# Optimization experiments

Measured on AMD Instinct MI355X. Metric: run time of the kernel, lower is better.

## Reference

```python
import jax, jax.numpy as jnp
import numpy as np

B = 32768      # batch of ODE state evaluations
N = 64         # input_size (number of variables / per-node MLPs)
H = 64         # hidden_size
N_DISCRETE = 16  # first 16 variables use straight-through gating
HIDDEN_FLAG = True


def setup_inputs() -> dict:
    key = jax.random.key(0)
    k1, k2, k3 = jax.random.split(key, 3)
    inputs = jax.random.normal(k1, (B, N), jnp.float32)
    # Stacked per-node MLP weights: net_i is Linear(N,H,bias=False) -> ReLU -> Linear(H,1,bias=False)
    W1 = jax.random.normal(k2, (N, H, N), jnp.float32) / np.sqrt(N).astype(np.float32)
    W2 = jax.random.normal(k3, (N, H), jnp.float32) / np.sqrt(H).astype(np.float32)
    adjacency = jnp.ones((N, N), jnp.float32)  # buffer, initialized to ones
    discrete_mask = jnp.arange(N) < N_DISCRETE  # bool [N], from input_type_list
    return {"t": 0, "inputs": inputs, "W1": W1, "W2": W2,
            "adjacency": adjacency, "discrete_mask": discrete_mask}


def reference(t, inputs, W1, W2, adjacency, discrete_mask):
    # Straight-through discrete gating: y_hard - sg(y_soft) + y_soft
    y_soft = jax.nn.sigmoid(inputs)
    st = (inputs > 0).astype(inputs.dtype) - jax.lax.stop_gradient(y_soft) + y_soft
    x = jnp.where(discrete_mask[None, :], st, inputs)  # [B, N]

    # Effective per-node input mask: row i of adjacency; last node additionally
    # filtered to only its own (hidden) feature when hidden_flag is set.
    M = adjacency
    if HIDDEN_FLAG:
        one_hot_last = jnp.zeros((N,), M.dtype).at[-1].set(1.0)
        M = M.at[-1].set(M[-1] * one_hot_last)

    # Masking the input of node i by M[i] is equivalent to masking W1[i]'s input dim.
    W1m = W1 * M[:, None, :]                      # [N, H, N]
    h = jax.nn.relu(jnp.einsum('bn,ihn->bih', x, W1m))  # [B, N, H]
    out = jnp.einsum('bih,ih->bi', h, W2)               # [B, N]
    return out
```

## Files before the change

kernel.cpp:

```cpp
#include <hip/hip_runtime.h>
#include <stdint.h>


typedef __attribute__((ext_vector_type(8))) short short8;
typedef __attribute__((ext_vector_type(4))) float floatx4;

#define NN 64
#define HH 64
#define BB 32768
#define OTW 33
#define X_ELEMS (BB * NN)
#define W1_ELEMS (NN * HH * NN)

__device__ __forceinline__ unsigned short f32_to_bf16_bits(float f) {
    union { float f; unsigned int i; } c; c.f = f;
    unsigned int b = c.i;
    b += 0x7fffu + ((b >> 16) & 1u);
    return (unsigned short)(b >> 16);
}

__device__ __forceinline__ bool sniff_bf16(const void* x) {
    const int lane = threadIdx.x & 63;
    const ushort* xw = (const ushort*)x;
    const ushort a = xw[4 * lane];
    const ushort b = xw[4 * lane + 2];
    const int ea = (a >> 7) & 0xFF, eb = (b >> 7) & 0xFF;
    const int hit = ((ea >= 118 && ea <= 132) ? 1 : 0) + ((eb >= 118 && eb <= 132) ? 1 : 0);
    const unsigned long long m1 = __ballot(hit >= 1);
    const unsigned long long m2 = __ballot(hit >= 2);
    return (__popcll(m1) + __popcll(m2)) >= 64;
}

__global__ __launch_bounds__(256, 4)
void prep_kernel(const void* __restrict__ x, const void* __restrict__ w1,
                 ushort* __restrict__ xo, ushort* __restrict__ w1o)
{
    const bool is_bf16 = sniff_bf16(x);
    const long base = ((long)blockIdx.x * 256 + (long)threadIdx.x) * 8;

    if (base < X_ELEMS) {
        const bool gate = (base & 63) < 16;
        short8 v;
        if (is_bf16) {
            v = *(const short8*)((const ushort*)x + base);
            if (gate) {
                #pragma unroll
                for (int j = 0; j < 8; ++j) {
                    const unsigned short u = (unsigned short)v[j];
                    const bool pos = ((u & 0x8000u) == 0) && ((u & 0x7fffu) != 0);
                    v[j] = pos ? (short)0x3F80 : (short)0;
                }
            }
        } else {
            const float* p = (const float*)x + base;
            const float4 f0 = *(const float4*)(p);
            const float4 f1 = *(const float4*)(p + 4);
            const float vals[8] = {f0.x, f0.y, f0.z, f0.w, f1.x, f1.y, f1.z, f1.w};
            #pragma unroll
            for (int j = 0; j < 8; ++j) {
                if (gate) v[j] = (vals[j] > 0.f) ? (short)0x3F80 : (short)0;
                else      v[j] = (short)f32_to_bf16_bits(vals[j]);
            }
        }
        *(short8*)(xo + base) = v;
    } else {
        const long wb = base - X_ELEMS;
        if (wb < W1_ELEMS) {
            short8 v;
            if (is_bf16) {
                v = *(const short8*)((const ushort*)w1 + wb);
            } else {
                const float* p = (const float*)w1 + wb;
                const float4 f0 = *(const float4*)(p);
                const float4 f1 = *(const float4*)(p + 4);
                const float vals[8] = {f0.x, f0.y, f0.z, f0.w, f1.x, f1.y, f1.z, f1.w};
                #pragma unroll
                for (int j = 0; j < 8; ++j) v[j] = (short)f32_to_bf16_bits(vals[j]);
            }
            const int node = (int)(wb >> 12);
            if (node == NN - 1) {
                const int w63 = (int)(wb & 63);
                #pragma unroll
                for (int j = 0; j < 8; ++j)
                    if (w63 + j != NN - 1) v[j] = 0;
            }
            *(short8*)(w1o + wb) = v;
        }
    }
}

template<bool F32>
__device__ __forceinline__ void main_body(const ushort* __restrict__ xo,
                                          const ushort* __restrict__ w1o,
                                          const void* __restrict__ w2p,
                                          void* __restrict__ outp,
                                          float* outTile)
{
    const int tid  = threadIdx.x;
    const int wave = tid >> 6;
    const int lane = tid & 63;
    const int quad = lane >> 4;
    const int l16  = lane & 15;

    const int blk   = blockIdx.x;
    const int b0    = (blk >> 1) * 64;
    const int nhalf = blk & 1;
    const int nbase = nhalf * 32 + wave * 8;

    short8 xfrag[2][4];
    #pragma unroll
    for (int ks = 0; ks < 2; ++ks)
        #pragma unroll
        for (int nt = 0; nt < 4; ++nt)
            xfrag[ks][nt] = *(const short8*)(xo + (b0 + nt * 16 + l16) * NN + ks * 32 + quad * 8);

    short8 w[2][4];
    auto loadW1mt = [&](int node, int mt) {
        const ushort* w1n = w1o + node * (HH * NN) + (mt * 16 + l16) * NN + quad * 8;
        w[0][mt] = *(const short8*)(w1n);
        w[1][mt] = *(const short8*)(w1n + 32);
    };

    #pragma unroll
    for (int mt = 0; mt < 4; ++mt) loadW1mt(nbase, mt);

    #pragma unroll 1
    for (int np = 0; np < 8; ++np) {
        const int node = nbase + np;
        const int nextnode = (np < 7) ? (node + 1) : node;

        float w2v[4][4];
        #pragma unroll
        for (int mt = 0; mt < 4; ++mt) {
            const int idx = node * HH + mt * 16 + quad * 4;
            if (F32) {
                const float4 ww = *(const float4*)((const float*)w2p + idx);
                w2v[mt][0] = ww.x; w2v[mt][1] = ww.y; w2v[mt][2] = ww.z; w2v[mt][3] = ww.w;
            } else {
                const ushort4 ww = *(const ushort4*)((const ushort*)w2p + idx);
                union { unsigned int i; float f; } c0, c1, c2, c3;
                c0.i = ((unsigned int)ww.x) << 16; c1.i = ((unsigned int)ww.y) << 16;
                c2.i = ((unsigned int)ww.z) << 16; c3.i = ((unsigned int)ww.w) << 16;
                w2v[mt][0] = c0.f; w2v[mt][1] = c1.f; w2v[mt][2] = c2.f; w2v[mt][3] = c3.f;
            }
        }

        float psum[4] = {0.f, 0.f, 0.f, 0.f};

        #pragma unroll
        for (int mt = 0; mt < 4; ++mt) {
            floatx4 acc[4];
            #pragma unroll
            for (int nt = 0; nt < 4; ++nt) acc[nt] = (floatx4){0.f, 0.f, 0.f, 0.f};
            #pragma unroll
            for (int ks = 0; ks < 2; ++ks)
                #pragma unroll
                for (int nt = 0; nt < 4; ++nt)
                    acc[nt] = __builtin_amdgcn_mfma_f32_16x16x32_bf16(
                        w[ks][mt], xfrag[ks][nt], acc[nt], 0, 0, 0);

            loadW1mt(nextnode, mt);

            #pragma unroll
            for (int nt = 0; nt < 4; ++nt) {
                float a0 = acc[nt][0]; a0 = a0 > 0.f ? a0 : 0.f;
                float a1 = acc[nt][1]; a1 = a1 > 0.f ? a1 : 0.f;
                float a2 = acc[nt][2]; a2 = a2 > 0.f ? a2 : 0.f;
                float a3 = acc[nt][3]; a3 = a3 > 0.f ? a3 : 0.f;
                float s0 = fmaf(a0, w2v[mt][0], psum[nt]);
                float s1 = a1 * w2v[mt][1];
                s0 = fmaf(a2, w2v[mt][2], s0);
                s1 = fmaf(a3, w2v[mt][3], s1);
                psum[nt] = s0 + s1;
            }
        }

        #pragma unroll
        for (int nt = 0; nt < 4; ++nt) {
            psum[nt] += __shfl_xor(psum[nt], 16, 64);
            psum[nt] += __shfl_xor(psum[nt], 32, 64);
        }

        const float val = (quad == 0) ? psum[0] : (quad == 1) ? psum[1]
                         : (quad == 2) ? psum[2] : psum[3];
        outTile[lane * OTW + (node & 31)] = val;
    }

    __syncthreads();

    const int row = tid >> 2;
    const int q   = tid & 3;
    const float* rp = outTile + row * OTW + q * 8;
    const size_t obase = (size_t)(b0 + row) * NN + nhalf * 32 + q * 8;
    if (F32) {
        float* op = (float*)outp + obase;
        *(float4*)(op)     = make_float4(rp[0], rp[1], rp[2], rp[3]);
        *(float4*)(op + 4) = make_float4(rp[4], rp[5], rp[6], rp[7]);
    } else {
        ushort* op = (ushort*)outp + obase;
        short8 o;
        #pragma unroll
        for (int c = 0; c < 8; ++c) o[c] = (short)f32_to_bf16_bits(rp[c]);
        *(short8*)(op) = o;
    }
}

__global__ __launch_bounds__(256, 4)
void main_kernel(const void* __restrict__ xorig,
                 const ushort* __restrict__ xo, const ushort* __restrict__ w1o,
                 const void* __restrict__ w2p, void* __restrict__ outp)
{
    __shared__ float outTile[64 * OTW];
    const bool is_bf16 = sniff_bf16(xorig);
    if (is_bf16) main_body<false>(xo, w1o, w2p, outp, outTile);
    else         main_body<true >(xo, w1o, w2p, outp, outTile);
}

#define LDSW 20
template<bool F32>
__device__ __forceinline__ void run_body_fb(const void* xp, const void* w1p,
                                            const void* w2p, void* outp,
                                            float* myLds)
{
    const int tid  = threadIdx.x;
    const int wave = tid >> 6;
    const int lane = tid & 63;
    const int quad = lane >> 4;
    const int l16  = lane & 15;
    const int blk  = blockIdx.x;
    const int ng   = blk >> 7;
    const int rbg  = blk & 127;
    const int node = ng * 4 + wave;
    const int rowbase = rbg * 256;

    short8 bfrag[2][4];
    #pragma unroll
    for (int ks = 0; ks < 2; ++ks) {
        #pragma unroll
        for (int ht = 0; ht < 4; ++ht) {
            const int h = ht * 16 + l16;
            const int k = ks * 32 + quad * 8;
            short8 v;
            if (F32) {
                const float* p = (const float*)w1p + node * (HH * NN) + h * NN + k;
                const float4 a0 = *(const float4*)(p);
                const float4 a1 = *(const float4*)(p + 4);
                const float vals[8] = {a0.x, a0.y, a0.z, a0.w, a1.x, a1.y, a1.z, a1.w};
                #pragma unroll
                for (int j = 0; j < 8; ++j) v[j] = (short)f32_to_bf16_bits(vals[j]);
            } else {
                v = *(const short8*)((const ushort*)w1p + node * (HH * NN) + h * NN + k);
            }
            if (node == NN - 1) {
                #pragma unroll
                for (int j = 0; j < 8; ++j)
                    if (k + j != NN - 1) v[j] = 0;
            }
            bfrag[ks][ht] = v;
        }
    }

    float w2reg[4];
    #pragma unroll
    for (int ht = 0; ht < 4; ++ht) {
        const int idx = node * HH + ht * 16 + l16;
        if (F32) {
            w2reg[ht] = ((const float*)w2p)[idx];
        } else {
            const ushort u = ((const ushort*)w2p)[idx];
            union { unsigned int i; float f; } cv; cv.i = ((unsigned int)u) << 16;
            w2reg[ht] = cv.f;
        }
    }

    #pragma unroll 1
    for (int it = 0; it < 4; ++it) {
        const int b0 = rowbase + it * 64;
        short8 afrag[2][4];
        #pragma unroll
        for (int ks = 0; ks < 2; ++ks) {
            #pragma unroll
            for (int rt = 0; rt < 4; ++rt) {
                const int rowg = b0 + rt * 16 + l16;
                const int k    = ks * 32 + quad * 8;
                const bool gate = (ks == 0 && quad < 2);
                short8 v;
                if (F32) {
                    const float* p = (const float*)xp + rowg * NN + k;
                    const float4 a0 = *(const float4*)(p);
                    const float4 a1 = *(const float4*)(p + 4);
                    const float vals[8] = {a0.x, a0.y, a0.z, a0.w, a1.x, a1.y, a1.z, a1.w};
                    #pragma unroll
                    for (int j = 0; j < 8; ++j) {
                        if (gate) v[j] = (vals[j] > 0.f) ? (short)0x3F80 : (short)0;
                        else      v[j] = (short)f32_to_bf16_bits(vals[j]);
                    }
                } else {
                    v = *(const short8*)((const ushort*)xp + rowg * NN + k);
                    if (gate) {
                        #pragma unroll
                        for (int j = 0; j < 8; ++j) {
                            const unsigned short u = (unsigned short)v[j];
                            const bool pos = ((u & 0x8000u) == 0) && ((u & 0x7fffu) != 0);
                            v[j] = pos ? (short)0x3F80 : (short)0;
                        }
                    }
                }
                afrag[ks][rt] = v;
            }
        }

        floatx4 acc[4][4];
        #pragma unroll
        for (int rt = 0; rt < 4; ++rt)
            #pragma unroll
            for (int ht = 0; ht < 4; ++ht)
                acc[rt][ht] = (floatx4){0.f, 0.f, 0.f, 0.f};
        #pragma unroll
        for (int ks = 0; ks < 2; ++ks)
            #pragma unroll
            for (int rt = 0; rt < 4; ++rt)
                #pragma unroll
                for (int ht = 0; ht < 4; ++ht)
                    acc[rt][ht] = __builtin_amdgcn_mfma_f32_16x16x32_bf16(
                        afrag[ks][rt], bfrag[ks][ht], acc[rt][ht], 0, 0, 0);

        #pragma unroll
        for (int rt = 0; rt < 4; ++rt) {
            #pragma unroll
            for (int r = 0; r < 4; ++r) {
                float s = 0.f;
                #pragma unroll
                for (int ht = 0; ht < 4; ++ht) {
                    float v = acc[rt][ht][r];
                    v = v > 0.f ? v : 0.f;
                    s = fmaf(v, w2reg[ht], s);
                }
                myLds[(rt * 16 + quad * 4 + r) * LDSW + l16] = s;
            }
        }
        __syncthreads();
        const float* rowp = myLds + lane * LDSW;
        const float4 v0 = *(const float4*)(rowp + 0);
        const float4 v1 = *(const float4*)(rowp + 4);
        const float4 v2 = *(const float4*)(rowp + 8);
        const float4 v3 = *(const float4*)(rowp + 12);
        const float tot = (((v0.x + v0.y) + (v0.z + v0.w)) + ((v1.x + v1.y) + (v1.z + v1.w)))
                        + (((v2.x + v2.y) + (v2.z + v2.w)) + ((v3.x + v3.y) + (v3.z + v3.w)));
        if (F32) ((float*) outp)[(size_t)(b0 + lane) * NN + node] = tot;
        else     ((ushort*)outp)[(size_t)(b0 + lane) * NN + node] = f32_to_bf16_bits(tot);
        __syncthreads();
    }
}

__global__ __launch_bounds__(256, 2)
void fallback_kernel(const void* __restrict__ x, const void* __restrict__ W1,
                     const void* __restrict__ W2, void* __restrict__ out)
{
    __shared__ float lds[4][64 * LDSW];
    const bool is_bf16 = sniff_bf16(x);
    float* myLds = &lds[threadIdx.x >> 6][0];
    if (is_bf16) run_body_fb<false>(x, W1, W2, out, myLds);
    else         run_body_fb<true >(x, W1, W2, out, myLds);
}

extern "C" void kernel_launch(void* const* d_in, const int* in_sizes, int n_in,
                              void* d_out, int out_size, void* d_ws, size_t ws_size,
                              hipStream_t stream) {
    int i_in = -1, i_w1 = -1, i_w2 = -1;
    for (int i = 0; i < n_in; ++i) {
        const int s = in_sizes[i];
        if      (s == BB * NN  && i_in < 0) i_in = i;
        else if (s == NN*HH*NN && i_w1 < 0) i_w1 = i;
        else if (s == NN*HH    && i_w2 < 0) i_w2 = i;
    }
    if (i_in < 0) i_in = (n_in > 1) ? 1 : 0;
    if (i_w1 < 0) i_w1 = i_in + 1;
    if (i_w2 < 0) i_w2 = i_w1 + 1;

    const size_t need = (size_t)(X_ELEMS + W1_ELEMS) * sizeof(ushort);
    if (ws_size >= need) {
        ushort* xo  = (ushort*)d_ws;
        ushort* w1o = xo + X_ELEMS;
        prep_kernel<<<dim3((X_ELEMS + W1_ELEMS) / (256 * 8)), dim3(256), 0, stream>>>(
            d_in[i_in], d_in[i_w1], xo, w1o);
        main_kernel<<<dim3(1024), dim3(256), 0, stream>>>(
            d_in[i_in], xo, w1o, d_in[i_w2], d_out);
    } else {
        fallback_kernel<<<dim3(16 * 128), dim3(256), 0, stream>>>(
            d_in[i_in], d_in[i_w1], d_in[i_w2], d_out);
    }
}
```

Measured before the change: 113.8 us.

## Fuse prep conversion into main kernel with LDS double-buffered W1 staging

Removes the separate prep kernel and workspace path, so the input gating and bf16 conversion of x and W1 happen inline in a single fused kernel. Each block now covers 256 batch rows by 8 nodes. Per-node W1 tiles are staged through swizzled, double-buffered LDS and shared by all four waves, and W2 is preloaded into LDS. This cuts one kernel launch and the round trip through a global workspace, in exchange for re-converting W1 per block (128 times) and syncing once per node.

```diff
diff --git a/kernel.cpp b/kernel.cpp
--- a/kernel.cpp
+++ b/kernel.cpp
@@ -8,9 +8,7 @@
 #define NN 64
 #define HH 64
 #define BB 32768
-#define OTW 33
-#define X_ELEMS (BB * NN)
-#define W1_ELEMS (NN * HH * NN)
+#define OTW 9
 
 __device__ __forceinline__ unsigned short f32_to_bf16_bits(float f) {
     union { float f; unsigned int i; } c; c.f = f;
@@ -31,69 +29,13 @@
     return (__popcll(m1) + __popcll(m2)) >= 64;
 }
 
-__global__ __launch_bounds__(256, 4)
-void prep_kernel(const void* __restrict__ x, const void* __restrict__ w1,
-                 ushort* __restrict__ xo, ushort* __restrict__ w1o)
-{
-    const bool is_bf16 = sniff_bf16(x);
-    const long base = ((long)blockIdx.x * 256 + (long)threadIdx.x) * 8;
-
-    if (base < X_ELEMS) {
-        const bool gate = (base & 63) < 16;
-        short8 v;
-        if (is_bf16) {
-            v = *(const short8*)((const ushort*)x + base);
-            if (gate) {
-                #pragma unroll
-                for (int j = 0; j < 8; ++j) {
-                    const unsigned short u = (unsigned short)v[j];
-                    const bool pos = ((u & 0x8000u) == 0) && ((u & 0x7fffu) != 0);
-                    v[j] = pos ? (short)0x3F80 : (short)0;
-                }
-            }
-        } else {
-            const float* p = (const float*)x + base;
-            const float4 f0 = *(const float4*)(p);
-            const float4 f1 = *(const float4*)(p + 4);
-            const float vals[8] = {f0.x, f0.y, f0.z, f0.w, f1.x, f1.y, f1.z, f1.w};
-            #pragma unroll
-            for (int j = 0; j < 8; ++j) {
-                if (gate) v[j] = (vals[j] > 0.f) ? (short)0x3F80 : (short)0;
-                else      v[j] = (short)f32_to_bf16_bits(vals[j]);
-            }
-        }
-        *(short8*)(xo + base) = v;
-    } else {
-        const long wb = base - X_ELEMS;
-        if (wb < W1_ELEMS) {
-            short8 v;
-            if (is_bf16) {
-                v = *(const short8*)((const ushort*)w1 + wb);
-            } else {
-                const float* p = (const float*)w1 + wb;
-                const float4 f0 = *(const float4*)(p);
-                const float4 f1 = *(const float4*)(p + 4);
-                const float vals[8] = {f0.x, f0.y, f0.z, f0.w, f1.x, f1.y, f1.z, f1.w};
-                #pragma unroll
-                for (int j = 0; j < 8; ++j) v[j] = (short)f32_to_bf16_bits(vals[j]);
-            }
-            const int node = (int)(wb >> 12);
-            if (node == NN - 1) {
-                const int w63 = (int)(wb & 63);
-                #pragma unroll
-                for (int j = 0; j < 8; ++j)
-                    if (w63 + j != NN - 1) v[j] = 0;
-            }
-            *(short8*)(w1o + wb) = v;
-        }
-    }
-}
-
 template<bool F32>
-__device__ __forceinline__ void main_body(const ushort* __restrict__ xo,
-                                          const ushort* __restrict__ w1o,
+__device__ __forceinline__ void main_body(const void* __restrict__ xp,
+                                          const void* __restrict__ w1p,
                                           const void* __restrict__ w2p,
                                           void* __restrict__ outp,
+                                          ushort (*w1st)[4096],
+                                          float* w2lds,
                                           float* outTile)
 {
     const int tid  = threadIdx.x;
@@ -102,53 +44,120 @@
     const int quad = lane >> 4;
     const int l16  = lane & 15;
 
-    const int blk   = blockIdx.x;
-    const int b0    = (blk >> 1) * 64;
-    const int nhalf = blk & 1;
-    const int nbase = nhalf * 32 + wave * 8;
+    const int blk = blockIdx.x;
+    const int b0  = (blk >> 3) * 256;
+    const int n0  = (blk & 7) * 8;
+    const int bw  = b0 + wave * 64;
+
+    if (tid < 128) {
+        const int i4 = tid * 4;
+        if (F32) {
+            *(float4*)(w2lds + i4) = *(const float4*)((const float*)w2p + n0 * HH + i4);
+        } else {
+            const ushort4 u = *(const ushort4*)((const ushort*)w2p + n0 * HH + i4);
+            union { unsigned int i; float f; } c;
+            c.i = ((unsigned int)u.x) << 16; w2lds[i4 + 0] = c.f;
+            c.i = ((unsigned int)u.y) << 16; w2lds[i4 + 1] = c.f;
+            c.i = ((unsigned int)u.z) << 16; w2lds[i4 + 2] = c.f;
+            c.i = ((unsigned int)u.w) << 16; w2lds[i4 + 3] = c.f;
+        }
+    }
 
     short8 xfrag[2][4];
     #pragma unroll
-    for (int ks = 0; ks < 2; ++ks)
-        #pragma unroll
-        for (int nt = 0; nt < 4; ++nt)
-            xfrag[ks][nt] = *(const short8*)(xo + (b0 + nt * 16 + l16) * NN + ks * 32 + quad * 8);
-
-    short8 w[2][4];
-    auto loadW1mt = [&](int node, int mt) {
-        const ushort* w1n = w1o + node * (HH * NN) + (mt * 16 + l16) * NN + quad * 8;
-        w[0][mt] = *(const short8*)(w1n);
-        w[1][mt] = *(const short8*)(w1n + 32);
+    for (int ks = 0; ks < 2; ++ks) {
+        #pragma unroll
+        for (int nt = 0; nt < 4; ++nt) {
+            const int rowg = bw + nt * 16 + l16;
+            const int k    = ks * 32 + quad * 8;
+            const bool gate = (ks == 0 && quad < 2);
+            short8 v;
+            if (F32) {
+                const float* p = (const float*)xp + (size_t)rowg * NN + k;
+                const float4 a0 = *(const float4*)(p);
+                const float4 a1 = *(const float4*)(p + 4);
+                const float vals[8] = {a0.x, a0.y, a0.z, a0.w, a1.x, a1.y, a1.z, a1.w};
+                #pragma unroll
+                for (int j = 0; j < 8; ++j) {
+                    if (gate) v[j] = (vals[j] > 0.f) ? (short)0x3F80 : (short)0;
+                    else      v[j] = (short)f32_to_bf16_bits(vals[j]);
+                }
+            } else {
+                v = *(const short8*)((const ushort*)xp + (size_t)rowg * NN + k);
+                if (gate) {
+                    #pragma unroll
+                    for (int j = 0; j < 8; ++j) {
+                        const unsigned short u = (unsigned short)v[j];
+                        const bool pos = ((u & 0x8000u) == 0) && ((u & 0x7fffu) != 0);
+                        v[j] = pos ? (short)0x3F80 : (short)0;
+                    }
+                }
+            }
+            xfrag[ks][nt] = v;
+        }
+    }
+
+    short8 sv[2];
+    auto stageLoad = [&](int node) {
+        #pragma unroll
+        for (int i = 0; i < 2; ++i) {
+            const int c = i * 256 + tid;
+            short8 v;
+            if (F32) {
+                const float* p = (const float*)w1p + (size_t)node * 4096 + c * 8;
+                const float4 a0 = *(const float4*)(p);
+                const float4 a1 = *(const float4*)(p + 4);
+                const float vals[8] = {a0.x, a0.y, a0.z, a0.w, a1.x, a1.y, a1.z, a1.w};
+                #pragma unroll
+                for (int j = 0; j < 8; ++j) v[j] = (short)f32_to_bf16_bits(vals[j]);
+            } else {
+                v = *(const short8*)((const ushort*)w1p + (size_t)node * 4096 + c * 8);
+            }
+            if (node == NN - 1) {
+                if ((c & 7) == 7) {
+                    #pragma unroll
+                    for (int j = 0; j < 7; ++j) v[j] = 0;
+                } else {
+                    v = (short8){0,0,0,0,0,0,0,0};
+                }
+            }
+            sv[i] = v;
+        }
     };
-
-    #pragma unroll
-    for (int mt = 0; mt < 4; ++mt) loadW1mt(nbase, mt);
+    auto stageWrite = [&](int cur) {
+        #pragma unroll
+        for (int i = 0; i < 2; ++i) {
+            const int c = i * 256 + tid;
+            const int p = c ^ ((c >> 3) & 7);
+            *(short8*)(&w1st[cur][0] + p * 8) = sv[i];
+        }
+    };
+
+    stageLoad(n0);
+    stageWrite(0);
+    __syncthreads();
 
     #pragma unroll 1
     for (int np = 0; np < 8; ++np) {
-        const int node = nbase + np;
-        const int nextnode = (np < 7) ? (node + 1) : node;
-
-        float w2v[4][4];
+        const int cur = np & 1;
+
+        if (np < 7) stageLoad(n0 + np + 1);
+
+        short8 w[2][4];
+        #pragma unroll
+        for (int ks = 0; ks < 2; ++ks) {
+            #pragma unroll
+            for (int mt = 0; mt < 4; ++mt) {
+                const int c = (mt * 16 + l16) * 8 + ks * 4 + quad;
+                const int p = c ^ ((c >> 3) & 7);
+                w[ks][mt] = *(const short8*)(&w1st[cur][0] + p * 8);
+            }
+        }
+
+        float psum[4] = {0.f, 0.f, 0.f, 0.f};
         #pragma unroll
         for (int mt = 0; mt < 4; ++mt) {
-            const int idx = node * HH + mt * 16 + quad * 4;
-            if (F32) {
-                const float4 ww = *(const float4*)((const float*)w2p + idx);
-                w2v[mt][0] = ww.x; w2v[mt][1] = ww.y; w2v[mt][2] = ww.z; w2v[mt][3] = ww.w;
-            } else {
-                const ushort4 ww = *(const ushort4*)((const ushort*)w2p + idx);
-                union { unsigned int i; float f; } c0, c1, c2, c3;
-                c0.i = ((unsigned int)ww.x) << 16; c1.i = ((unsigned int)ww.y) << 16;
-                c2.i = ((unsigned int)ww.z) << 16; c3.i = ((unsigned int)ww.w) << 16;
-                w2v[mt][0] = c0.f; w2v[mt][1] = c1.f; w2v[mt][2] = c2.f; w2v[mt][3] = c3.f;
-            }
-        }
-
-        float psum[4] = {0.f, 0.f, 0.f, 0.f};
-
-        #pragma unroll
-        for (int mt = 0; mt < 4; ++mt) {
+            const float4 ww = *(const float4*)(w2lds + np * HH + mt * 16 + quad * 4);
             floatx4 acc[4];
             #pragma unroll
             for (int nt = 0; nt < 4; ++nt) acc[nt] = (floatx4){0.f, 0.f, 0.f, 0.f};
@@ -158,19 +167,16 @@
                 for (int nt = 0; nt < 4; ++nt)
                     acc[nt] = __builtin_amdgcn_mfma_f32_16x16x32_bf16(
                         w[ks][mt], xfrag[ks][nt], acc[nt], 0, 0, 0);
-
-            loadW1mt(nextnode, mt);
-
             #pragma unroll
             for (int nt = 0; nt < 4; ++nt) {
                 float a0 = acc[nt][0]; a0 = a0 > 0.f ? a0 : 0.f;
                 float a1 = acc[nt][1]; a1 = a1 > 0.f ? a1 : 0.f;
                 float a2 = acc[nt][2]; a2 = a2 > 0.f ? a2 : 0.f;
                 float a3 = acc[nt][3]; a3 = a3 > 0.f ? a3 : 0.f;
-                float s0 = fmaf(a0, w2v[mt][0], psum[nt]);
-                float s1 = a1 * w2v[mt][1];
-                s0 = fmaf(a2, w2v[mt][2], s0);
-                s1 = fmaf(a3, w2v[mt][3], s1);
+                float s0 = fmaf(a0, ww.x, psum[nt]);
+                float s1 = a1 * ww.y;
+                s0 = fmaf(a2, ww.z, s0);
+                s1 = fmaf(a3, ww.w, s1);
                 psum[nt] = s0 + s1;
             }
         }
@@ -183,15 +189,14 @@
 
         const float val = (quad == 0) ? psum[0] : (quad == 1) ? psum[1]
                          : (quad == 2) ? psum[2] : psum[3];
-        outTile[lane * OTW + (node & 31)] = val;
-    }
-
-    __syncthreads();
-
-    const int row = tid >> 2;
-    const int q   = tid & 3;
-    const float* rp = outTile + row * OTW + q * 8;
-    const size_t obase = (size_t)(b0 + row) * NN + nhalf * 32 + q * 8;
+        outTile[(wave * 64 + lane) * OTW + np] = val;
+
+        if (np < 7) stageWrite(cur ^ 1);
+        __syncthreads();
+    }
+
+    const float* rp = outTile + tid * OTW;
+    const size_t obase = (size_t)(b0 + tid) * NN + n0;
     if (F32) {
         float* op = (float*)outp + obase;
         *(float4*)(op)     = make_float4(rp[0], rp[1], rp[2], rp[3]);
@@ -206,162 +211,15 @@
 }
 
 __global__ __launch_bounds__(256, 4)
-void main_kernel(const void* __restrict__ xorig,
-                 const ushort* __restrict__ xo, const ushort* __restrict__ w1o,
+void main_kernel(const void* __restrict__ x, const void* __restrict__ w1p,
                  const void* __restrict__ w2p, void* __restrict__ outp)
 {
-    __shared__ float outTile[64 * OTW];
-    const bool is_bf16 = sniff_bf16(xorig);
-    if (is_bf16) main_body<false>(xo, w1o, w2p, outp, outTile);
-    else         main_body<true >(xo, w1o, w2p, outp, outTile);
-}
-
-#define LDSW 20
-template<bool F32>
-__device__ __forceinline__ void run_body_fb(const void* xp, const void* w1p,
-                                            const void* w2p, void* outp,
-                                            float* myLds)
-{
-    const int tid  = threadIdx.x;
-    const int wave = tid >> 6;
-    const int lane = tid & 63;
-    const int quad = lane >> 4;
-    const int l16  = lane & 15;
-    const int blk  = blockIdx.x;
-    const int ng   = blk >> 7;
-    const int rbg  = blk & 127;
-    const int node = ng * 4 + wave;
-    const int rowbase = rbg * 256;
-
-    short8 bfrag[2][4];
-    #pragma unroll
-    for (int ks = 0; ks < 2; ++ks) {
-        #pragma unroll
-        for (int ht = 0; ht < 4; ++ht) {
-            const int h = ht * 16 + l16;
-            const int k = ks * 32 + quad * 8;
-            short8 v;
-            if (F32) {
-                const float* p = (const float*)w1p + node * (HH * NN) + h * NN + k;
-                const float4 a0 = *(const float4*)(p);
-                const float4 a1 = *(const float4*)(p + 4);
-                const float vals[8] = {a0.x, a0.y, a0.z, a0.w, a1.x, a1.y, a1.z, a1.w};
-                #pragma unroll
-                for (int j = 0; j < 8; ++j) v[j] = (short)f32_to_bf16_bits(vals[j]);
-            } else {
-                v = *(const short8*)((const ushort*)w1p + node * (HH * NN) + h * NN + k);
-            }
-            if (node == NN - 1) {
-                #pragma unroll
-                for (int j = 0; j < 8; ++j)
-                    if (k + j != NN - 1) v[j] = 0;
-            }
-            bfrag[ks][ht] = v;
-        }
-    }
-
-    float w2reg[4];
-    #pragma unroll
-    for (int ht = 0; ht < 4; ++ht) {
-        const int idx = node * HH + ht * 16 + l16;
-        if (F32) {
-            w2reg[ht] = ((const float*)w2p)[idx];
-        } else {
-            const ushort u = ((const ushort*)w2p)[idx];
-            union { unsigned int i; float f; } cv; cv.i = ((unsigned int)u) << 16;
-            w2reg[ht] = cv.f;
-        }
-    }
-
-    #pragma unroll 1
-    for (int it = 0; it < 4; ++it) {
-        const int b0 = rowbase + it * 64;
-        short8 afrag[2][4];
-        #pragma unroll
-        for (int ks = 0; ks < 2; ++ks) {
-            #pragma unroll
-            for (int rt = 0; rt < 4; ++rt) {
-                const int rowg = b0 + rt * 16 + l16;
-                const int k    = ks * 32 + quad * 8;
-                const bool gate = (ks == 0 && quad < 2);
-                short8 v;
-                if (F32) {
-                    const float* p = (const float*)xp + rowg * NN + k;
-                    const float4 a0 = *(const float4*)(p);
-                    const float4 a1 = *(const float4*)(p + 4);
-                    const float vals[8] = {a0.x, a0.y, a0.z, a0.w, a1.x, a1.y, a1.z, a1.w};
-                    #pragma unroll
-                    for (int j = 0; j < 8; ++j) {
-                        if (gate) v[j] = (vals[j] > 0.f) ? (short)0x3F80 : (short)0;
-                        else      v[j] = (short)f32_to_bf16_bits(vals[j]);
-                    }
-                } else {
-                    v = *(const short8*)((const ushort*)xp + rowg * NN + k);
-                    if (gate) {
-                        #pragma unroll
-                        for (int j = 0; j < 8; ++j) {
-                            const unsigned short u = (unsigned short)v[j];
-                            const bool pos = ((u & 0x8000u) == 0) && ((u & 0x7fffu) != 0);
-                            v[j] = pos ? (short)0x3F80 : (short)0;
-                        }
-                    }
-                }
-                afrag[ks][rt] = v;
-            }
-        }
-
-        floatx4 acc[4][4];
-        #pragma unroll
-        for (int rt = 0; rt < 4; ++rt)
-            #pragma unroll
-            for (int ht = 0; ht < 4; ++ht)
-                acc[rt][ht] = (floatx4){0.f, 0.f, 0.f, 0.f};
-        #pragma unroll
-        for (int ks = 0; ks < 2; ++ks)
-            #pragma unroll
-            for (int rt = 0; rt < 4; ++rt)
-                #pragma unroll
-                for (int ht = 0; ht < 4; ++ht)
-                    acc[rt][ht] = __builtin_amdgcn_mfma_f32_16x16x32_bf16(
-                        afrag[ks][rt], bfrag[ks][ht], acc[rt][ht], 0, 0, 0);
-
-        #pragma unroll
-        for (int rt = 0; rt < 4; ++rt) {
-            #pragma unroll
-            for (int r = 0; r < 4; ++r) {
-                float s = 0.f;
-                #pragma unroll
-                for (int ht = 0; ht < 4; ++ht) {
-                    float v = acc[rt][ht][r];
-                    v = v > 0.f ? v : 0.f;
-                    s = fmaf(v, w2reg[ht], s);
-                }
-                myLds[(rt * 16 + quad * 4 + r) * LDSW + l16] = s;
-            }
-        }
-        __syncthreads();
-        const float* rowp = myLds + lane * LDSW;
-        const float4 v0 = *(const float4*)(rowp + 0);
-        const float4 v1 = *(const float4*)(rowp + 4);
-        const float4 v2 = *(const float4*)(rowp + 8);
-        const float4 v3 = *(const float4*)(rowp + 12);
-        const float tot = (((v0.x + v0.y) + (v0.z + v0.w)) + ((v1.x + v1.y) + (v1.z + v1.w)))
-                        + (((v2.x + v2.y) + (v2.z + v2.w)) + ((v3.x + v3.y) + (v3.z + v3.w)));
-        if (F32) ((float*) outp)[(size_t)(b0 + lane) * NN + node] = tot;
-        else     ((ushort*)outp)[(size_t)(b0 + lane) * NN + node] = f32_to_bf16_bits(tot);
-        __syncthreads();
-    }
-}
-
-__global__ __launch_bounds__(256, 2)
-void fallback_kernel(const void* __restrict__ x, const void* __restrict__ W1,
-                     const void* __restrict__ W2, void* __restrict__ out)
-{
-    __shared__ float lds[4][64 * LDSW];
+    __shared__ ushort w1st[2][4096];
+    __shared__ float  w2lds[8 * HH];
+    __shared__ float  outTile[256 * OTW];
     const bool is_bf16 = sniff_bf16(x);
-    float* myLds = &lds[threadIdx.x >> 6][0];
-    if (is_bf16) run_body_fb<false>(x, W1, W2, out, myLds);
-    else         run_body_fb<true >(x, W1, W2, out, myLds);
+    if (is_bf16) main_body<false>(x, w1p, w2p, outp, w1st, w2lds, outTile);
+    else         main_body<true >(x, w1p, w2p, outp, w1st, w2lds, outTile);
 }
 
 extern "C" void kernel_launch(void* const* d_in, const int* in_sizes, int n_in,
@@ -378,16 +236,7 @@
     if (i_w1 < 0) i_w1 = i_in + 1;
     if (i_w2 < 0) i_w2 = i_w1 + 1;
 
-    const size_t need = (size_t)(X_ELEMS + W1_ELEMS) * sizeof(ushort);
-    if (ws_size >= need) {
-        ushort* xo  = (ushort*)d_ws;
-        ushort* w1o = xo + X_ELEMS;
-        prep_kernel<<<dim3((X_ELEMS + W1_ELEMS) / (256 * 8)), dim3(256), 0, stream>>>(
-            d_in[i_in], d_in[i_w1], xo, w1o);
-        main_kernel<<<dim3(1024), dim3(256), 0, stream>>>(
-            d_in[i_in], xo, w1o, d_in[i_w2], d_out);
-    } else {
-        fallback_kernel<<<dim3(16 * 128), dim3(256), 0, stream>>>(
-            d_in[i_in], d_in[i_w1], d_in[i_w2], d_out);
-    }
-}
+    (void)d_ws; (void)ws_size;
+    main_kernel<<<dim3(1024), dim3(256), 0, stream>>>(
+        d_in[i_in], d_in[i_w1], d_in[i_w2], d_out);
+}
```

New measurement: 102.9 us. 9.6% less time.
